# Optimization experiments

Hardware: AMD Instinct MI355X
Metric: run time of the kernel (lower is better)

The kernel has to match this reference:

```python
import jax, jax.numpy as jnp
import numpy as np

P_FACTOR = 3.0
EPS = 1e-12  # matches torch F.normalize clamp_min eps


def _normalize(x):
    # L2-normalize along the feature (last) axis, like F.normalize(x, dim=1) on 2D
    n = jnp.sqrt(jnp.sum(x * x, axis=-1, keepdims=True))
    return x / jnp.maximum(n, EPS)


def setup_inputs() -> dict:
    key = jax.random.key(0)
    ks = jax.random.split(key, 7)
    N, M, F, E = 8192, 16384, 768, 512
    X = jax.random.normal(ks[0], (N, F), dtype=jnp.float32)
    D = jax.random.normal(ks[1], (M, F), dtype=jnp.float32)
    r = jax.random.uniform(ks[2], (M, 1), dtype=jnp.float32)
    g_w = jax.random.normal(ks[3], (E, F), dtype=jnp.float32) * (1.0 / np.sqrt(F))
    g_b = jax.random.normal(ks[4], (E,), dtype=jnp.float32) * 0.01
    h_w = jax.random.normal(ks[5], (1, 1), dtype=jnp.float32)
    h_b = jax.random.normal(ks[6], (1,), dtype=jnp.float32) * 0.01
    return {"X": X, "D": D, "r": r, "g_w": g_w, "g_b": g_b, "h_w": h_w, "h_b": h_b}


def reference(X, D, r, g_w, g_b, h_w, h_b):
    # r = r * 2 - 1  (map [0,1] correctness labels to [-1,1])
    r2 = r * 2.0 - 1.0
    # g: shared linear embedding of queries and exemplars
    Xg = X @ g_w.T + g_b          # [N, E]
    Dg = D @ g_w.T + g_b          # [M, E]
    # Minerva: cosine similarity
    a = _normalize(Xg) @ _normalize(Dg).T   # [N, M]
    # power-sign activation: |a|^p * sign(a)
    a = jnp.power(jnp.abs(a), P_FACTOR) * jnp.sign(a)
    # echo = weighted sum of exemplar labels
    echo = a @ r2                 # [N, 1]
    # h: Linear(1,1) then sigmoid
    out = jax.nn.sigmoid(echo @ h_w.T + h_b)  # [N, 1]
    return out
```

## Files before the change

### kernel.cpp

```cpp
#include <hip/hip_runtime.h>
#include <stdint.h>

#define F_DIM 768
#define E_DIM 512

typedef __attribute__((ext_vector_type(4))) float f32x4;
typedef __attribute__((ext_vector_type(8))) __bf16 bf16x8;

__device__ __forceinline__ uint16_t f2bf(float f) {
  uint32_t u = __builtin_bit_cast(uint32_t, f);
  return (uint16_t)((u + 0x7FFFu + ((u >> 16) & 1u)) >> 16);
}

#define GLOAD_LDS16(g, l) __builtin_amdgcn_global_load_lds(                 \
    (const __attribute__((address_space(1))) void*)(g),                     \
    (__attribute__((address_space(3))) void*)(l), 16, 0, 0)

__global__ __launch_bounds__(256) void embed_gemm(
    const float* __restrict__ src, const float* __restrict__ gw,
    const float* __restrict__ gb, uint16_t* __restrict__ out) {
  __shared__ uint4 smem4[2048];
  char* smc = (char*)smem4;
  const int t = threadIdx.x;
  const int l = t & 63, w = t >> 6, wm = w >> 1, wn = w & 1;
  const int bx = blockIdx.x, by = blockIdx.y;
  const int g = l >> 4, x7 = l & 7;

  f32x4 acc[4][4];
#pragma unroll
  for (int a_ = 0; a_ < 4; ++a_)
#pragma unroll
    for (int b_ = 0; b_ < 4; ++b_) acc[a_][b_] = (f32x4){0.f, 0.f, 0.f, 0.f};

  const int rr0 = t >> 3;
  const int ss  = t & 7;

  for (int kk = 0; kk < F_DIM; kk += 64) {
    __syncthreads();
#pragma unroll
    for (int c = 0; c < 4; ++c) {
      const int rr = c * 32 + rr0;
      const int wb = rr * 128 + ((ss ^ (rr & 7)) << 4);
      {
        const float* p = src + (size_t)(bx * 128 + rr) * F_DIM + kk + ss * 8;
        float4 lo = *(const float4*)p;
        float4 hi = *(const float4*)(p + 4);
        uint4 pk;
        pk.x = f2bf(lo.x) | ((uint32_t)f2bf(lo.y) << 16);
        pk.y = f2bf(lo.z) | ((uint32_t)f2bf(lo.w) << 16);
        pk.z = f2bf(hi.x) | ((uint32_t)f2bf(hi.y) << 16);
        pk.w = f2bf(hi.z) | ((uint32_t)f2bf(hi.w) << 16);
        *(uint4*)(smc + wb) = pk;
      }
      {
        const float* p = gw + (size_t)(by * 128 + rr) * F_DIM + kk + ss * 8;
        float4 lo = *(const float4*)p;
        float4 hi = *(const float4*)(p + 4);
        uint4 pk;
        pk.x = f2bf(lo.x) | ((uint32_t)f2bf(lo.y) << 16);
        pk.y = f2bf(lo.z) | ((uint32_t)f2bf(lo.w) << 16);
        pk.z = f2bf(hi.x) | ((uint32_t)f2bf(hi.y) << 16);
        pk.w = f2bf(hi.z) | ((uint32_t)f2bf(hi.w) << 16);
        *(uint4*)(smc + 16384 + wb) = pk;
      }
    }
    __syncthreads();
#pragma unroll
    for (int ks = 0; ks < 2; ++ks) {
      const int slotoff = ((ks * 4 + g) ^ x7) << 4;
      bf16x8 af[4], bfr[4];
#pragma unroll
      for (int fm = 0; fm < 4; ++fm)
        af[fm] = *(const bf16x8*)(smc + (wm * 64 + fm * 16 + (l & 15)) * 128 + slotoff);
#pragma unroll
      for (int fn = 0; fn < 4; ++fn)
        bfr[fn] = *(const bf16x8*)(smc + 16384 + (wn * 64 + fn * 16 + (l & 15)) * 128 + slotoff);
#pragma unroll
      for (int fm = 0; fm < 4; ++fm)
#pragma unroll
        for (int fn = 0; fn < 4; ++fn)
          acc[fm][fn] = __builtin_amdgcn_mfma_f32_16x16x32_bf16(
              af[fm], bfr[fn], acc[fm][fn], 0, 0, 0);
    }
  }

  const int colb = by * 128 + wn * 64;
#pragma unroll
  for (int fn = 0; fn < 4; ++fn) {
    const int col = colb + fn * 16 + (l & 15);
    const float bias = gb[col];
#pragma unroll
    for (int fm = 0; fm < 4; ++fm) {
      const int rowb = bx * 128 + wm * 64 + fm * 16 + g * 4;
#pragma unroll
      for (int v = 0; v < 4; ++v)
        out[(size_t)(rowb + v) * E_DIM + col] = f2bf(acc[fm][fn][v] + bias);
    }
  }
}

__global__ __launch_bounds__(256) void l2norm_rows(uint16_t* __restrict__ eg) {
  const int row = blockIdx.x * 4 + (threadIdx.x >> 6);
  const int l = threadIdx.x & 63;
  uint16_t* p = eg + (size_t)row * E_DIM + l * 8;
  uint4 v = *(const uint4*)p;
  uint32_t wd[4] = {v.x, v.y, v.z, v.w};
  float f[8];
#pragma unroll
  for (int i = 0; i < 4; ++i) {
    f[2 * i]     = __builtin_bit_cast(float, (wd[i] & 0xFFFFu) << 16);
    f[2 * i + 1] = __builtin_bit_cast(float, wd[i] & 0xFFFF0000u);
  }
  float s = 0.f;
#pragma unroll
  for (int i = 0; i < 8; ++i) s += f[i] * f[i];
#pragma unroll
  for (int m = 1; m < 64; m <<= 1) s += __shfl_xor(s, m);
  const float inv = 1.0f / fmaxf(sqrtf(s), 1e-12f);
  uint4 o;
  o.x = f2bf(f[0] * inv) | ((uint32_t)f2bf(f[1] * inv) << 16);
  o.y = f2bf(f[2] * inv) | ((uint32_t)f2bf(f[3] * inv) << 16);
  o.z = f2bf(f[4] * inv) | ((uint32_t)f2bf(f[5] * inv) << 16);
  o.w = f2bf(f[6] * inv) | ((uint32_t)f2bf(f[7] * inv) << 16);
  *(uint4*)p = o;
}

__global__ __launch_bounds__(256) void minerva_main(
    const uint16_t* __restrict__ Xn, const uint16_t* __restrict__ Dn,
    const float* __restrict__ rin, float* __restrict__ echo) {
  __shared__ uint4 smem4[2048];
  char* smc = (char*)smem4;
  const int t = threadIdx.x;
  const int l = t & 63, w = t >> 6, wm = w >> 1, wn = w & 1;
  const int bx = blockIdx.x, by = blockIdx.y;
  const int g = l >> 4, x7 = l & 7;

  f32x4 acc[4][4];
#pragma unroll
  for (int a_ = 0; a_ < 4; ++a_)
#pragma unroll
    for (int b_ = 0; b_ < 4; ++b_) acc[a_][b_] = (f32x4){0.f, 0.f, 0.f, 0.f};

  const int rr0 = t >> 3, ss = t & 7;
  const int s0 = ss ^ (rr0 & 7);
  const uint16_t* pA = Xn + (size_t)(bx * 128 + rr0) * E_DIM + s0 * 8;
  const uint16_t* pB = Dn + (size_t)(by * 128 + rr0) * E_DIM + s0 * 8;
  char* ldsA = smc + t * 16;
  char* ldsB = smc + 16384 + t * 16;

  for (int kk = 0; kk < E_DIM; kk += 64) {
    __syncthreads();
#pragma unroll
    for (int i = 0; i < 4; ++i) {
      GLOAD_LDS16(pA + (size_t)i * 32 * E_DIM + kk, ldsA + i * 4096);
      GLOAD_LDS16(pB + (size_t)i * 32 * E_DIM + kk, ldsB + i * 4096);
    }
    __syncthreads();
#pragma unroll
    for (int ks = 0; ks < 2; ++ks) {
      const int slotoff = ((ks * 4 + g) ^ x7) << 4;
      bf16x8 af[4], bfr[4];
#pragma unroll
      for (int fm = 0; fm < 4; ++fm)
        af[fm] = *(const bf16x8*)(smc + (wm * 64 + fm * 16 + (l & 15)) * 128 + slotoff);
#pragma unroll
      for (int fn = 0; fn < 4; ++fn)
        bfr[fn] = *(const bf16x8*)(smc + 16384 + (wn * 64 + fn * 16 + (l & 15)) * 128 + slotoff);
#pragma unroll
      for (int fm = 0; fm < 4; ++fm)
#pragma unroll
        for (int fn = 0; fn < 4; ++fn)
          acc[fm][fn] = __builtin_amdgcn_mfma_f32_16x16x32_bf16(
              af[fm], bfr[fn], acc[fm][fn], 0, 0, 0);
    }
  }

  const int jb = by * 128 + wn * 64;
  float r2[4];
#pragma unroll
  for (int fn = 0; fn < 4; ++fn)
    r2[fn] = rin[jb + fn * 16 + (l & 15)] * 2.0f - 1.0f;
  const int rowb = bx * 128 + wm * 64;
#pragma unroll
  for (int fm = 0; fm < 4; ++fm) {
#pragma unroll
    for (int v = 0; v < 4; ++v) {
      float sum = 0.f;
#pragma unroll
      for (int fn = 0; fn < 4; ++fn) {
        const float a = acc[fm][fn][v];
        sum += a * a * a * r2[fn];
      }
      sum += __shfl_xor(sum, 1);
      sum += __shfl_xor(sum, 2);
      sum += __shfl_xor(sum, 4);
      sum += __shfl_xor(sum, 8);
      if ((l & 15) == 0)
        atomicAdd(&echo[rowb + fm * 16 + g * 4 + v], sum);
    }
  }
}

__global__ __launch_bounds__(256) void head_sigmoid(
    const float* __restrict__ echo, const float* __restrict__ hw,
    const float* __restrict__ hb, float* __restrict__ out, int n) {
  const int i = blockIdx.x * 256 + threadIdx.x;
  if (i < n) {
    const float e = echo[i] * hw[0] + hb[0];
    out[i] = 1.0f / (1.0f + __expf(-e));
  }
}

extern "C" void kernel_launch(void* const* d_in, const int* in_sizes, int n_in,
                              void* d_out, int out_size, void* d_ws, size_t ws_size,
                              hipStream_t stream) {
  const float* X  = (const float*)d_in[0];
  const float* D  = (const float*)d_in[1];
  const float* r  = (const float*)d_in[2];
  const float* gw = (const float*)d_in[3];
  const float* gb = (const float*)d_in[4];
  const float* hw = (const float*)d_in[5];
  const float* hb = (const float*)d_in[6];
  float* out = (float*)d_out;
  const int N = in_sizes[0] / F_DIM;
  const int M = in_sizes[1] / F_DIM;

  uint16_t* Xn = (uint16_t*)d_ws;
  uint16_t* Dn = Xn + (size_t)N * E_DIM;
  float* echo = (float*)((char*)d_ws + (size_t)(N + M) * E_DIM * 2);

  hipMemsetAsync(echo, 0, (size_t)N * sizeof(float), stream);

  dim3 blk(256);
  embed_gemm<<<dim3(N / 128, E_DIM / 128), blk, 0, stream>>>(X, gw, gb, Xn);
  embed_gemm<<<dim3(M / 128, E_DIM / 128), blk, 0, stream>>>(D, gw, gb, Dn);
  l2norm_rows<<<(N + M) / 4, blk, 0, stream>>>(Xn);
  minerva_main<<<dim3(N / 128, M / 128), blk, 0, stream>>>(Xn, Dn, r, echo);
  head_sigmoid<<<(N + 255) / 256, blk, 0, stream>>>(echo, hw, hb, out, N);
}
```

Baseline: 360.0 us.

## Enlarge similarity GEMM tile to 256x256 with double-buffered LDS pipelining

Rewrites the main cosine-similarity GEMM to use 256x256 output tiles with 512 threads (8 waves, each computing 128x64) instead of 128x128 with 256 threads. The K loop becomes a double-buffered LDS pipeline: direct global-to-LDS loads for the next K tile are interleaved with MFMA phases, with split barriers and s_setprio to raise MFMA priority. This aims to increase data reuse per LDS byte, cut the atomic traffic on echo, and hide load latency. The cost is 128KB of dynamic LDS per block and more accumulator registers, which may limit occupancy to one block per CU.

```diff
diff --git a/kernel.cpp b/kernel.cpp
--- a/kernel.cpp
+++ b/kernel.cpp
@@ -125,64 +125,87 @@
   *(uint4*)p = o;
 }
 
-__global__ __launch_bounds__(256) void minerva_main(
+__global__ __launch_bounds__(512, 2) void minerva_main256(
     const uint16_t* __restrict__ Xn, const uint16_t* __restrict__ Dn,
     const float* __restrict__ rin, float* __restrict__ echo) {
-  __shared__ uint4 smem4[2048];
-  char* smc = (char*)smem4;
-  const int t = threadIdx.x;
-  const int l = t & 63, w = t >> 6, wm = w >> 1, wn = w & 1;
+  extern __shared__ __align__(16) char smem[];
+  const int t_ = threadIdx.x;
+  const int l = t_ & 63, w = t_ >> 6;
+  const int wm = w >> 2, wn = w & 3;
   const int bx = blockIdx.x, by = blockIdx.y;
-  const int g = l >> 4, x7 = l & 7;
-
-  f32x4 acc[4][4];
-#pragma unroll
-  for (int a_ = 0; a_ < 4; ++a_)
+  const int g = l >> 4, x7 = l & 7, l15 = l & 15;
+
+  f32x4 acc[8][4];
+#pragma unroll
+  for (int a_ = 0; a_ < 8; ++a_)
 #pragma unroll
     for (int b_ = 0; b_ < 4; ++b_) acc[a_][b_] = (f32x4){0.f, 0.f, 0.f, 0.f};
 
-  const int rr0 = t >> 3, ss = t & 7;
-  const int s0 = ss ^ (rr0 & 7);
-  const uint16_t* pA = Xn + (size_t)(bx * 128 + rr0) * E_DIM + s0 * 8;
-  const uint16_t* pB = Dn + (size_t)(by * 128 + rr0) * E_DIM + s0 * 8;
-  char* ldsA = smc + t * 16;
-  char* ldsB = smc + 16384 + t * 16;
-
-  for (int kk = 0; kk < E_DIM; kk += 64) {
-    __syncthreads();
-#pragma unroll
-    for (int i = 0; i < 4; ++i) {
-      GLOAD_LDS16(pA + (size_t)i * 32 * E_DIM + kk, ldsA + i * 4096);
-      GLOAD_LDS16(pB + (size_t)i * 32 * E_DIM + kk, ldsB + i * 4096);
-    }
-    __syncthreads();
-#pragma unroll
-    for (int ks = 0; ks < 2; ++ks) {
-      const int slotoff = ((ks * 4 + g) ^ x7) << 4;
-      bf16x8 af[4], bfr[4];
-#pragma unroll
-      for (int fm = 0; fm < 4; ++fm)
-        af[fm] = *(const bf16x8*)(smc + (wm * 64 + fm * 16 + (l & 15)) * 128 + slotoff);
-#pragma unroll
-      for (int fn = 0; fn < 4; ++fn)
-        bfr[fn] = *(const bf16x8*)(smc + 16384 + (wn * 64 + fn * 16 + (l & 15)) * 128 + slotoff);
-#pragma unroll
-      for (int fm = 0; fm < 4; ++fm)
-#pragma unroll
-        for (int fn = 0; fn < 4; ++fn)
-          acc[fm][fn] = __builtin_amdgcn_mfma_f32_16x16x32_bf16(
-              af[fm], bfr[fn], acc[fm][fn], 0, 0, 0);
-    }
-  }
-
-  const int jb = by * 128 + wn * 64;
+  const int rr = t_ >> 3, ss = t_ & 7;
+  const int s0 = ss ^ (rr & 7);
+  const uint16_t* gA = Xn + (size_t)(bx * 256 + rr) * E_DIM + s0 * 8;
+  const uint16_t* gB = Dn + (size_t)(by * 256 + rr) * E_DIM + s0 * 8;
+  char* ldsDst = smem + t_ * 16;
+
+#define STG_A(CUR, KK, I) GLOAD_LDS16(gA + (size_t)(I) * 64 * E_DIM + (KK), \
+                                      ldsDst + (CUR) * 32768 + (I) * 8192)
+#define STG_B(CUR, KK, I) GLOAD_LDS16(gB + (size_t)(I) * 64 * E_DIM + (KK), \
+                                      ldsDst + 65536 + (CUR) * 32768 + (I) * 8192)
+
+#define PHASE(FM0, KS, READ_B, GL, LAST)                                       \
+  {                                                                            \
+    const int so = (((KS) * 4 + g) ^ x7) << 4;                                 \
+    bf16x8 af[4];                                                              \
+    _Pragma("unroll") for (int i_ = 0; i_ < 4; ++i_)                           \
+        af[i_] = *(const bf16x8*)(bufA +                                       \
+                  (wm * 128 + ((FM0) + i_) * 16 + l15) * 128 + so);            \
+    if (READ_B) {                                                              \
+      _Pragma("unroll") for (int j_ = 0; j_ < 4; ++j_)                         \
+          bfr[j_] = *(const bf16x8*)(bufB +                                    \
+                    (wn * 64 + j_ * 16 + l15) * 128 + so);                     \
+    }                                                                          \
+    GL;                                                                        \
+    __builtin_amdgcn_s_barrier();                                              \
+    __builtin_amdgcn_s_setprio(1);                                             \
+    _Pragma("unroll") for (int i_ = 0; i_ < 4; ++i_)                           \
+        _Pragma("unroll") for (int j_ = 0; j_ < 4; ++j_)                       \
+            acc[(FM0) + i_][j_] = __builtin_amdgcn_mfma_f32_16x16x32_bf16(     \
+                af[i_], bfr[j_], acc[(FM0) + i_][j_], 0, 0, 0);                \
+    __builtin_amdgcn_s_setprio(0);                                             \
+    if (LAST) asm volatile("s_waitcnt vmcnt(0)" ::: "memory");                 \
+    __builtin_amdgcn_s_barrier();                                              \
+  }
+
+#define TILE(KKN, CUR, PF)                                                     \
+  {                                                                            \
+    char* bufA = smem + (CUR) * 32768;                                         \
+    char* bufB = smem + 65536 + (CUR) * 32768;                                 \
+    bf16x8 bfr[4];                                                             \
+    PHASE(0, 0, 1, if (PF) { STG_A(1 - (CUR), KKN, 0); STG_A(1 - (CUR), KKN, 1); }, 0) \
+    PHASE(4, 0, 0, if (PF) { STG_A(1 - (CUR), KKN, 2); STG_A(1 - (CUR), KKN, 3); }, 0) \
+    PHASE(0, 1, 1, if (PF) { STG_B(1 - (CUR), KKN, 0); STG_B(1 - (CUR), KKN, 1); }, 0) \
+    PHASE(4, 1, 0, if (PF) { STG_B(1 - (CUR), KKN, 2); STG_B(1 - (CUR), KKN, 3); }, 1) \
+  }
+
+  STG_A(0, 0, 0); STG_A(0, 0, 1); STG_A(0, 0, 2); STG_A(0, 0, 3);
+  STG_B(0, 0, 0); STG_B(0, 0, 1); STG_B(0, 0, 2); STG_B(0, 0, 3);
+  asm volatile("s_waitcnt vmcnt(0)" ::: "memory");
+  __builtin_amdgcn_s_barrier();
+
+  for (int t2 = 0; t2 < 8; t2 += 2) {
+    TILE((t2 + 1) * 64, 0, 1);
+    const int pf2 = (t2 < 6);
+    TILE((t2 + 2) * 64, 1, pf2);
+  }
+
+  const int jb = by * 256 + wn * 64;
   float r2[4];
 #pragma unroll
   for (int fn = 0; fn < 4; ++fn)
-    r2[fn] = rin[jb + fn * 16 + (l & 15)] * 2.0f - 1.0f;
-  const int rowb = bx * 128 + wm * 64;
-#pragma unroll
-  for (int fm = 0; fm < 4; ++fm) {
+    r2[fn] = rin[jb + fn * 16 + l15] * 2.0f - 1.0f;
+  const int rowb = bx * 256 + wm * 128;
+#pragma unroll
+  for (int fm = 0; fm < 8; ++fm) {
 #pragma unroll
     for (int v = 0; v < 4; ++v) {
       float sum = 0.f;
@@ -195,10 +218,14 @@
       sum += __shfl_xor(sum, 2);
       sum += __shfl_xor(sum, 4);
       sum += __shfl_xor(sum, 8);
-      if ((l & 15) == 0)
+      if (l15 == 0)
         atomicAdd(&echo[rowb + fm * 16 + g * 4 + v], sum);
     }
   }
+#undef STG_A
+#undef STG_B
+#undef PHASE
+#undef TILE
 }
 
 __global__ __launch_bounds__(256) void head_sigmoid(
@@ -231,10 +258,13 @@
 
   hipMemsetAsync(echo, 0, (size_t)N * sizeof(float), stream);
 
+  (void)hipFuncSetAttribute((const void*)minerva_main256,
+                            hipFuncAttributeMaxDynamicSharedMemorySize, 131072);
+
   dim3 blk(256);
   embed_gemm<<<dim3(N / 128, E_DIM / 128), blk, 0, stream>>>(X, gw, gb, Xn);
   embed_gemm<<<dim3(M / 128, E_DIM / 128), blk, 0, stream>>>(D, gw, gb, Dn);
   l2norm_rows<<<(N + M) / 4, blk, 0, stream>>>(Xn);
-  minerva_main<<<dim3(N / 128, M / 128), blk, 0, stream>>>(Xn, Dn, r, echo);
+  minerva_main256<<<dim3(N / 256, M / 256), dim3(512), 131072, stream>>>(Xn, Dn, r, echo);
   head_sigmoid<<<(N + 255) / 256, blk, 0, stream>>>(echo, hw, hb, out, N);
 }
```

New measurement: 330.5 us. 1.09x faster.
